# Performance work log

Measured on AMD Instinct MI355X. Metric: run time of the kernel, lower is better.

Reference implementation:

```python
import jax, jax.numpy as jnp
import numpy as np

LN_ZERO = -100000000000.0
F_, D_, C_, V_ = 250000, 4, 2, 250000
E_ = F_ * D_
CD_ = C_ ** D_


def setup_inputs() -> dict:
    key = jax.random.key(0)
    k1, k2, k3 = jax.random.split(key, 3)
    # each factor has exactly D_ incident edges, one per variable slot
    edge_f = np.repeat(np.arange(E_ // D_ * 0 + F_ * 0 + F_)[:F_], D_)  # [E]
    pos = np.tile(np.arange(D_), F_)  # variable slot of each edge within its factor
    edge_v = np.asarray(jax.random.randint(k3, (E_,), 0, V_))
    # digit of each flat factor state along each axis: digits[k, s] in [0, C)
    state = np.arange(CD_)
    digits = (state[None, :] // (C_ ** (D_ - 1 - np.arange(D_)))[:, None]) % C_  # [D, CD]
    s_p = digits[pos]  # [E, CD]: the edge's own variable state within each factor state
    # permutation indices into the broadcast-first layout [E, C, C^(D-1)]
    scatter_idx = (np.arange(E_)[:, None] * CD_ + s_p * C_ ** (D_ - 1)).reshape(-1)
    fac_states_to_var = (np.arange(E_)[:, None] * C_ + s_p).reshape(-1)
    return {
        "prv_factorToVar_messages": jax.random.normal(k1, (E_, C_), jnp.float32),
        "factor_potentials": jax.random.normal(k2, (F_,) + (C_,) * D_, jnp.float32),
        "facToVar_edge_idx": jnp.asarray(np.stack([edge_f, edge_v]), jnp.int32),
        "facStates_to_varIdx": jnp.asarray(fac_states_to_var, jnp.int32),
        "varToFactorMsg_scatter_indices": jnp.asarray(scatter_idx, jnp.int32),
        "factor_potential_masks": jnp.zeros((F_,) + (C_,) * D_, jnp.int32),
        "factorToVar_messages_masks": jnp.zeros((E_, C_), bool),
        "varToFactor_messages_masks": jnp.zeros((E_, C_), bool),
        "var_beliefs_masks": jnp.zeros((V_, C_), bool),
    }


def _mask_clamp(x, mask):
    return jnp.maximum(jnp.where(mask, LN_ZERO, x), LN_ZERO)


def reference(prv_factorToVar_messages, factor_potentials, facToVar_edge_idx,
              facStates_to_varIdx, varToFactorMsg_scatter_indices,
              factor_potential_masks, factorToVar_messages_masks,
              varToFactor_messages_masks, var_beliefs_masks):
    E, C = prv_factorToVar_messages.shape
    F = factor_potentials.shape[0]
    V = var_beliefs_masks.shape[0]
    D = factor_potentials.ndim - 1
    edge_f, edge_v = facToVar_edge_idx[0], facToVar_edge_idx[1]

    def beliefs(msgs):
        vb = _mask_clamp(jax.ops.segment_sum(msgs, edge_v, num_segments=V), var_beliefs_masks)
        v2f = _mask_clamp(vb[edge_v] - msgs, varToFactor_messages_masks)
        # expanded[e, s] = v2f[e, s_p]; source is broadcast layout [E, C, C^(D-1)]
        expanded = v2f.reshape(-1)[varToFactorMsg_scatter_indices // (C ** (D - 1))]
        expanded = expanded.reshape((E,) + (C,) * D)
        fb = jax.ops.segment_sum(expanded.reshape(E, -1), edge_f, num_segments=F)
        fb = fb.reshape(factor_potentials.shape) + factor_potentials
        fb = jnp.maximum(jnp.where(factor_potential_masks == 1, LN_ZERO, fb), LN_ZERO)
        return vb, v2f, expanded, fb

    prv_vb, prv_v2f, exp_prv_v2f, prv_fb = beliefs(prv_factorToVar_messages)

    # new factor->var messages: max-marginalize (mode='map')
    nfv = prv_fb[edge_f] - exp_prv_v2f
    nfv = nfv - jnp.max(nfv)
    flat = nfv.reshape(-1)
    seg = jnp.where(facStates_to_varIdx >= 0, facStates_to_varIdx, E * C)  # invalid -> dropped slot
    new_f2v = jax.ops.segment_max(flat, seg, num_segments=E * C + 1)[:-1].reshape(E, C)
    # normalization: logsumexp over all dims except dim 0 (here just the state axis)
    new_f2v = new_f2v - jax.nn.logsumexp(new_f2v, axis=1, keepdims=True)
    new_f2v = _mask_clamp(new_f2v, factorToVar_messages_masks)

    vb, v2f, _, fb = beliefs(new_f2v)

    damping = 0.0
    f2v = _mask_clamp(damping * prv_factorToVar_messages + (1.0 - damping) * new_f2v,
                      factorToVar_messages_masks)
    return (f2v, vb, fb)
```

## Files before the change

### kernel.cpp

```cpp
#include <hip/hip_runtime.h>
#include <hip/hip_fp16.h>
#include <math.h>
#include <string.h>

#define LN_ZERO (-100000000000.0f)

constexpr int F_ = 250000;
constexpr int V_ = 250000;
constexpr int E_ = 1000000;

constexpr int NBLK  = 256;
constexpr int PARTS = 256;
constexpr int BINS  = 977;
constexpr int CAP   = 30;
constexpr int SLICE = 3908;
constexpr int OVF_B = 1024;
constexpr int NWAVE = 16;
static_assert(PARTS * BINS >= V_, "");
static_assert((size_t)NBLK * SLICE >= E_, "");
static_assert(SLICE % 4 == 0, "");
static_assert(CAP <= 64, "segment items must fit one wave");
static_assert((size_t)NBLK * PARTS * CAP * 8 <= (size_t)F_ * 16 * 4, "buckets fit in out_fb");

static __device__ inline unsigned pack_h2(float x, float y) {
    __half2 h = __floats2half2_rn(x, y);
    unsigned u; memcpy(&u, &h, 4); return u;
}
static __device__ inline float2 unpack_h2(unsigned u) {
    __half2 h; memcpy(&h, &u, 4); return __half22float2(h);
}

__global__ __launch_bounds__(1024)
void k_ms1(const int* __restrict__ edge_v,
           const float2* __restrict__ msgs,
           const int4* __restrict__ potmask4,
           unsigned short* __restrict__ potbits,
           uint2* __restrict__ buckets,
           int* __restrict__ counts,
           uint2* __restrict__ ovf,
           int* __restrict__ ovf_counts) {
    __shared__ int cur[PARTS];
    __shared__ int ovf_cur;
    int b = blockIdx.x, tid = threadIdx.x;
    if (tid < PARTS) cur[tid] = 0;
    if (tid == 0) ovf_cur = 0;
    __syncthreads();

    int f = b * 1024 + tid;
    if (f < F_) {
        unsigned int bits = 0;
#pragma unroll
        for (int j = 0; j < 4; ++j) {
            int4 pm = potmask4[4 * f + j];
            bits |= (pm.x == 1 ? 1u : 0u) << (4 * j + 0);
            bits |= (pm.y == 1 ? 1u : 0u) << (4 * j + 1);
            bits |= (pm.z == 1 ? 1u : 0u) << (4 * j + 2);
            bits |= (pm.w == 1 ? 1u : 0u) << (4 * j + 3);
        }
        potbits[f] = (unsigned short)bits;
    }

    int ebase = b * SLICE;
    int eend = min(ebase + SLICE, E_);
    for (int e = ebase + tid; e < eend; e += 1024) {
        int v = edge_v[e];
        int p = v / BINS;
        float2 m = msgs[e];
        unsigned payload = pack_h2(m.x, m.y);
        int pos = atomicAdd(&cur[p], 1);
        if (pos < CAP) {
            buckets[((size_t)b * PARTS + p) * CAP + pos] =
                make_uint2((unsigned)(v - p * BINS), payload);
        } else {
            int op = atomicAdd(&ovf_cur, 1);
            if (op < OVF_B)
                ovf[(size_t)b * OVF_B + op] = make_uint2((unsigned)v, payload);
        }
    }
    __syncthreads();
    if (tid < PARTS) counts[tid * NBLK + b] = min(cur[tid], CAP);
    if (tid == 0) ovf_counts[b] = min(ovf_cur, OVF_B);
}

__global__ __launch_bounds__(1024)
void k_acc1(const uint2* __restrict__ buckets,
            const int* __restrict__ counts,
            const uint2* __restrict__ ovf,
            const int* __restrict__ ovf_counts,
            const unsigned short* __restrict__ vb_mask2,
            __half2* __restrict__ accP) {
    __shared__ float2 acc[BINS];
    __shared__ int ls_cnt[NBLK];
    __shared__ int ovfc[NBLK];
    int p = blockIdx.x, tid = threadIdx.x;
    int vbase = p * BINS;
    int nb = min(BINS, V_ - vbase);

    for (int j = tid; j < BINS; j += 1024) acc[j] = make_float2(0.f, 0.f);
    if (tid < NBLK) { ls_cnt[tid] = counts[p * NBLK + tid]; ovfc[tid] = ovf_counts[tid]; }
    __syncthreads();

    int wave = tid >> 6, lane = tid & 63;
    for (int b = wave; b < NBLK; b += NWAVE) {
        int n = ls_cnt[b];
        if (lane < n) {
            uint2 pr = buckets[((size_t)b * PARTS + p) * CAP + lane];
            float2 mv = unpack_h2(pr.y);
            atomicAdd(&acc[pr.x].x, mv.x);
            atomicAdd(&acc[pr.x].y, mv.y);
        }
    }
    for (int b = wave; b < NBLK; b += NWAVE) {
        int n = ovfc[b];
        for (int i = lane; i < n; i += 64) {
            uint2 pr = ovf[(size_t)b * OVF_B + i];
            int vl = (int)pr.x - vbase;
            if ((unsigned)vl < (unsigned)nb) {
                float2 mv = unpack_h2(pr.y);
                atomicAdd(&acc[vl].x, mv.x);
                atomicAdd(&acc[vl].y, mv.y);
            }
        }
    }
    __syncthreads();
    for (int j = tid; j < nb; j += 1024) {
        int v = vbase + j;
        unsigned short vbm = vb_mask2[v];
        float b0 = fmaxf((vbm & 0xff) ? LN_ZERO : acc[j].x, LN_ZERO);
        float b1 = fmaxf((vbm >> 8)   ? LN_ZERO : acc[j].y, LN_ZERO);
        accP[v] = __floats2half2_rn(b0, b1);
    }
}

__global__ __launch_bounds__(1024)
void k_fm_ms2(const float2* __restrict__ msgs,
              const int* __restrict__ edge_v,
              const __half2* __restrict__ accP,
              const float4* __restrict__ pot4,
              const unsigned short* __restrict__ potbits,
              const unsigned short* __restrict__ f2v_mask2,
              const unsigned short* __restrict__ v2f_mask2,
              float2* __restrict__ out_f2v,
              uint2* __restrict__ buckets,
              int* __restrict__ counts,
              uint2* __restrict__ ovf,
              int* __restrict__ ovf_counts) {
    __shared__ int cur[PARTS];
    __shared__ int ovf_cur;
    int b = blockIdx.x, tid = threadIdx.x;
    if (tid < PARTS) cur[tid] = 0;
    if (tid == 0) ovf_cur = 0;
    __syncthreads();

    int ebase = b * SLICE;
    int eend = min(ebase + SLICE, E_);
    for (int e = ebase + tid; e < eend; e += 1024) {
        int d = e & 3;
        int v = edge_v[e];

        float2 s = __half22float2(accP[v]);
        float2 m = msgs[e];
        unsigned short vm = v2f_mask2[e];
        float wx = fmaxf((vm & 0xff) ? LN_ZERO : (s.x - m.x), LN_ZERO);
        float wy = fmaxf((vm >> 8)   ? LN_ZERO : (s.y - m.y), LN_ZERO);

        float w0x = __shfl(wx, 0, 4), w0y = __shfl(wy, 0, 4);
        float w1x = __shfl(wx, 1, 4), w1y = __shfl(wy, 1, 4);
        float w2x = __shfl(wx, 2, 4), w2y = __shfl(wy, 2, 4);
        float w3x = __shfl(wx, 3, 4), w3y = __shfl(wy, 3, 4);

        float4 p = pot4[e];
        unsigned int pb = potbits[e >> 2] >> (4 * d);
        float A = ((d >> 1) ? w0y : w0x) + ((d & 1) ? w1y : w1x);
        float fb0 = p.x + A + w2x + w3x;
        float fb1 = p.y + A + w2x + w3y;
        float fb2 = p.z + A + w2y + w3x;
        float fb3 = p.w + A + w2y + w3y;
        fb0 = fmaxf((pb & 1u) ? LN_ZERO : fb0, LN_ZERO);
        fb1 = fmaxf((pb & 2u) ? LN_ZERO : fb1, LN_ZERO);
        fb2 = fmaxf((pb & 4u) ? LN_ZERO : fb2, LN_ZERO);
        fb3 = fmaxf((pb & 8u) ? LN_ZERO : fb3, LN_ZERO);

        float mk2_0 = fmaxf(fb0, fb1);
        float mk2_1 = fmaxf(fb2, fb3);
        float mk3_0 = fmaxf(fb0, fb2);
        float mk3_1 = fmaxf(fb1, fb3);
        float mloc  = fmaxf(mk2_0, mk2_1);

#pragma unroll
        for (int off = 1; off < 4; off <<= 1) {
            mk2_0 = fmaxf(mk2_0, __shfl_xor(mk2_0, off, 4));
            mk2_1 = fmaxf(mk2_1, __shfl_xor(mk2_1, off, 4));
            mk3_0 = fmaxf(mk3_0, __shfl_xor(mk3_0, off, 4));
            mk3_1 = fmaxf(mk3_1, __shfl_xor(mk3_1, off, 4));
        }
        float ml0 = __shfl(mloc, 0, 4);
        float ml1 = __shfl(mloc, 1, 4);
        float ml2 = __shfl(mloc, 2, 4);
        float ml3 = __shfl(mloc, 3, 4);

        float mm0, mm1;
        if (d == 0)      { mm0 = fmaxf(ml0, ml1); mm1 = fmaxf(ml2, ml3); }
        else if (d == 1) { mm0 = fmaxf(ml0, ml2); mm1 = fmaxf(ml1, ml3); }
        else if (d == 2) { mm0 = mk2_0;           mm1 = mk2_1; }
        else             { mm0 = mk3_0;           mm1 = mk3_1; }

        float raw0 = mm0 - wx;
        float raw1 = mm1 - wy;
        float mx = fmaxf(raw0, raw1);
        float lse = mx + logf(expf(raw0 - mx) + expf(raw1 - mx));
        unsigned short fm = f2v_mask2[e];
        float o0 = fmaxf((fm & 0xff) ? LN_ZERO : (raw0 - lse), LN_ZERO);
        float o1 = fmaxf((fm >> 8)   ? LN_ZERO : (raw1 - lse), LN_ZERO);
        out_f2v[e] = make_float2(o0, o1);

        int pp = v / BINS;
        unsigned payload = pack_h2(o0, o1);
        int pos = atomicAdd(&cur[pp], 1);
        if (pos < CAP) {
            buckets[((size_t)b * PARTS + pp) * CAP + pos] =
                make_uint2((unsigned)(v - pp * BINS), payload);
        } else {
            int op = atomicAdd(&ovf_cur, 1);
            if (op < OVF_B)
                ovf[(size_t)b * OVF_B + op] = make_uint2((unsigned)v, payload);
        }
    }
    __syncthreads();
    if (tid < PARTS) counts[tid * NBLK + b] = min(cur[tid], CAP);
    if (tid == 0) ovf_counts[b] = min(ovf_cur, OVF_B);
}

__global__ __launch_bounds__(1024)
void k_acc2(const uint2* __restrict__ buckets,
            const int* __restrict__ counts,
            const uint2* __restrict__ ovf,
            const int* __restrict__ ovf_counts,
            const unsigned short* __restrict__ vb_mask2,
            float2* __restrict__ out_vb,
            __half2* __restrict__ accN) {
    __shared__ float2 acc[BINS];
    __shared__ int ls_cnt[NBLK];
    __shared__ int ovfc[NBLK];
    int p = blockIdx.x, tid = threadIdx.x;
    int vbase = p * BINS;
    int nb = min(BINS, V_ - vbase);

    for (int j = tid; j < BINS; j += 1024) acc[j] = make_float2(0.f, 0.f);
    if (tid < NBLK) { ls_cnt[tid] = counts[p * NBLK + tid]; ovfc[tid] = ovf_counts[tid]; }
    __syncthreads();

    int wave = tid >> 6, lane = tid & 63;
    for (int b = wave; b < NBLK; b += NWAVE) {
        int n = ls_cnt[b];
        if (lane < n) {
            uint2 pr = buckets[((size_t)b * PARTS + p) * CAP + lane];
            float2 mv = unpack_h2(pr.y);
            atomicAdd(&acc[pr.x].x, mv.x);
            atomicAdd(&acc[pr.x].y, mv.y);
        }
    }
    for (int b = wave; b < NBLK; b += NWAVE) {
        int n = ovfc[b];
        for (int i = lane; i < n; i += 64) {
            uint2 pr = ovf[(size_t)b * OVF_B + i];
            int vl = (int)pr.x - vbase;
            if ((unsigned)vl < (unsigned)nb) {
                float2 mv = unpack_h2(pr.y);
                atomicAdd(&acc[vl].x, mv.x);
                atomicAdd(&acc[vl].y, mv.y);
            }
        }
    }
    __syncthreads();
    for (int j = tid; j < nb; j += 1024) {
        int v = vbase + j;
        unsigned short vbm = vb_mask2[v];
        float b0 = fmaxf((vbm & 0xff) ? LN_ZERO : acc[j].x, LN_ZERO);
        float b1 = fmaxf((vbm >> 8)   ? LN_ZERO : acc[j].y, LN_ZERO);
        out_vb[v] = make_float2(b0, b1);
        accN[v] = __floats2half2_rn(b0, b1);
    }
}

__global__ void k_factor_beliefs(const float2* __restrict__ new_f2v,
                                 const __half2* __restrict__ accN,
                                 const int* __restrict__ edge_v,
                                 const float4* __restrict__ pot4,
                                 const unsigned short* __restrict__ potbits,
                                 const unsigned short* __restrict__ v2f_mask2,
                                 float4* __restrict__ out_fb4) {
    int e = blockIdx.x * blockDim.x + threadIdx.x;
    if (e >= E_) return;
    int d = e & 3;

    float2 b = __half22float2(accN[edge_v[e]]);
    float2 g = new_f2v[e];
    unsigned short vm = v2f_mask2[e];
    float wx = fmaxf((vm & 0xff) ? LN_ZERO : (b.x - g.x), LN_ZERO);
    float wy = fmaxf((vm >> 8)   ? LN_ZERO : (b.y - g.y), LN_ZERO);

    float w0x = __shfl(wx, 0, 4), w0y = __shfl(wy, 0, 4);
    float w1x = __shfl(wx, 1, 4), w1y = __shfl(wy, 1, 4);
    float w2x = __shfl(wx, 2, 4), w2y = __shfl(wy, 2, 4);
    float w3x = __shfl(wx, 3, 4), w3y = __shfl(wy, 3, 4);

    float4 p = pot4[e];
    unsigned int pb = potbits[e >> 2] >> (4 * d);
    float A = ((d >> 1) ? w0y : w0x) + ((d & 1) ? w1y : w1x);
    float o0 = fmaxf((pb & 1u) ? LN_ZERO : (p.x + A + w2x + w3x), LN_ZERO);
    float o1 = fmaxf((pb & 2u) ? LN_ZERO : (p.y + A + w2x + w3y), LN_ZERO);
    float o2 = fmaxf((pb & 4u) ? LN_ZERO : (p.z + A + w2y + w3x), LN_ZERO);
    float o3 = fmaxf((pb & 8u) ? LN_ZERO : (p.w + A + w2y + w3y), LN_ZERO);
    out_fb4[e] = make_float4(o0, o1, o2, o3);
}

extern "C" void kernel_launch(void* const* d_in, const int* in_sizes, int n_in,
                              void* d_out, int out_size, void* d_ws, size_t ws_size,
                              hipStream_t stream) {
    const float* msgs     = (const float*)d_in[0];
    const float* pot      = (const float*)d_in[1];
    const int*   edge_idx = (const int*)d_in[2];
    const int*   pot_mask = (const int*)d_in[5];
    const unsigned char* f2v_mask = (const unsigned char*)d_in[6];
    const unsigned char* v2f_mask = (const unsigned char*)d_in[7];
    const unsigned char* vb_mask  = (const unsigned char*)d_in[8];

    const int* edge_v = edge_idx + E_;

    float* out      = (float*)d_out;
    float* out_f2v  = out;
    float* out_vb   = out + (size_t)E_ * 2;
    float* out_fb   = out_vb + (size_t)V_ * 2;

    uint2* buckets = (uint2*)out_fb;

    int* counts = (int*)d_ws;
    int* ovf_counts = counts + NBLK * PARTS;
    uint2* ovf = (uint2*)(ovf_counts + NBLK);
    __half2* accP = (__half2*)(ovf + (size_t)NBLK * OVF_B);
    __half2* accN = accP + V_;
    unsigned short* potbits = (unsigned short*)(accN + V_);

    const int B = 256;
    dim3 gE((E_ + B - 1) / B);

    k_ms1<<<NBLK, 1024, 0, stream>>>(edge_v, (const float2*)msgs,
                                     (const int4*)pot_mask, potbits,
                                     buckets, counts, ovf, ovf_counts);
    k_acc1<<<PARTS, 1024, 0, stream>>>(buckets, counts, ovf, ovf_counts,
                                       (const unsigned short*)vb_mask, accP);

    k_fm_ms2<<<NBLK, 1024, 0, stream>>>((const float2*)msgs, edge_v, accP,
                                        (const float4*)pot, potbits,
                                        (const unsigned short*)f2v_mask,
                                        (const unsigned short*)v2f_mask,
                                        (float2*)out_f2v,
                                        buckets, counts, ovf, ovf_counts);

    k_acc2<<<PARTS, 1024, 0, stream>>>(buckets, counts, ovf, ovf_counts,
                                       (const unsigned short*)vb_mask,
                                       (float2*)out_vb, accN);

    k_factor_beliefs<<<gE, B, 0, stream>>>((const float2*)out_f2v, accN, edge_v,
                                           (const float4*)pot, potbits,
                                           (const unsigned short*)v2f_mask,
                                           (float4*)out_fb);
}
```

Measured before the change: 75.00 us.

## Fuse five kernel launches into one cooperative kernel with grid syncs

Merges the scatter, accumulate, max-marginal, second accumulate, and factor-belief kernels into a single cooperative launch of 256 blocks of 1024 threads, with grid.sync between phases. The goal is to remove per-launch overhead and the gaps between dependent kernels. In exchange, the final factor-belief phase now runs on a fixed 256K-thread grid-stride loop instead of its own grid. Grid-wide barriers also add cost, and the launch depends on all 256 blocks being co-resident.

```diff
diff --git a/kernel.cpp b/kernel.cpp
--- a/kernel.cpp
+++ b/kernel.cpp
@@ -1,7 +1,10 @@
 #include <hip/hip_runtime.h>
+#include <hip/hip_cooperative_groups.h>
 #include <hip/hip_fp16.h>
 #include <math.h>
 #include <string.h>
+
+namespace cg = cooperative_groups;
 
 #define LN_ZERO (-100000000000.0f)
 
@@ -16,6 +19,7 @@
 constexpr int SLICE = 3908;
 constexpr int OVF_B = 1024;
 constexpr int NWAVE = 16;
+constexpr int NTHREADS = NBLK * 1024;
 static_assert(PARTS * BINS >= V_, "");
 static_assert((size_t)NBLK * SLICE >= E_, "");
 static_assert(SLICE % 4 == 0, "");
@@ -31,288 +35,260 @@
 }
 
 __global__ __launch_bounds__(1024)
-void k_ms1(const int* __restrict__ edge_v,
+void k_all(const int* __restrict__ edge_v,
            const float2* __restrict__ msgs,
            const int4* __restrict__ potmask4,
-           unsigned short* __restrict__ potbits,
-           uint2* __restrict__ buckets,
+           const float4* __restrict__ pot4,
+           const unsigned short* __restrict__ f2v_mask2,
+           const unsigned short* __restrict__ v2f_mask2,
+           const unsigned short* __restrict__ vb_mask2,
+           float2* __restrict__ out_f2v,
+           float2* __restrict__ out_vb,
+           float4* out_fb4,
+           uint2* buckets,
            int* __restrict__ counts,
            uint2* __restrict__ ovf,
-           int* __restrict__ ovf_counts) {
-    __shared__ int cur[PARTS];
-    __shared__ int ovf_cur;
-    int b = blockIdx.x, tid = threadIdx.x;
-    if (tid < PARTS) cur[tid] = 0;
-    if (tid == 0) ovf_cur = 0;
+           int* __restrict__ ovf_counts,
+           __half2* __restrict__ accP,
+           __half2* __restrict__ accN,
+           unsigned short* __restrict__ potbits) {
+    cg::grid_group grid = cg::this_grid();
+
+    __shared__ float2 s_acc[BINS];
+    __shared__ int s_ls[NBLK];
+    __shared__ int s_ovfc[NBLK];
+    __shared__ int s_cur[PARTS];
+    __shared__ int s_ovfcur;
+
+    const int b = blockIdx.x, tid = threadIdx.x;
+    const int wave = tid >> 6, lane = tid & 63;
+    const int ebase = b * SLICE;
+    const int eend = min(ebase + SLICE, E_);
+
+    if (tid < PARTS) s_cur[tid] = 0;
+    if (tid == 0) s_ovfcur = 0;
     __syncthreads();
 
-    int f = b * 1024 + tid;
-    if (f < F_) {
-        unsigned int bits = 0;
+    {
+        int f = b * 1024 + tid;
+        if (f < F_) {
+            unsigned int bits = 0;
 #pragma unroll
-        for (int j = 0; j < 4; ++j) {
-            int4 pm = potmask4[4 * f + j];
-            bits |= (pm.x == 1 ? 1u : 0u) << (4 * j + 0);
-            bits |= (pm.y == 1 ? 1u : 0u) << (4 * j + 1);
-            bits |= (pm.z == 1 ? 1u : 0u) << (4 * j + 2);
-            bits |= (pm.w == 1 ? 1u : 0u) << (4 * j + 3);
-        }
-        potbits[f] = (unsigned short)bits;
-    }
-
-    int ebase = b * SLICE;
-    int eend = min(ebase + SLICE, E_);
-    for (int e = ebase + tid; e < eend; e += 1024) {
-        int v = edge_v[e];
-        int p = v / BINS;
-        float2 m = msgs[e];
-        unsigned payload = pack_h2(m.x, m.y);
-        int pos = atomicAdd(&cur[p], 1);
-        if (pos < CAP) {
-            buckets[((size_t)b * PARTS + p) * CAP + pos] =
-                make_uint2((unsigned)(v - p * BINS), payload);
-        } else {
-            int op = atomicAdd(&ovf_cur, 1);
-            if (op < OVF_B)
-                ovf[(size_t)b * OVF_B + op] = make_uint2((unsigned)v, payload);
-        }
-    }
+            for (int j = 0; j < 4; ++j) {
+                int4 pm = potmask4[4 * f + j];
+                bits |= (pm.x == 1 ? 1u : 0u) << (4 * j + 0);
+                bits |= (pm.y == 1 ? 1u : 0u) << (4 * j + 1);
+                bits |= (pm.z == 1 ? 1u : 0u) << (4 * j + 2);
+                bits |= (pm.w == 1 ? 1u : 0u) << (4 * j + 3);
+            }
+            potbits[f] = (unsigned short)bits;
+        }
+        for (int e = ebase + tid; e < eend; e += 1024) {
+            int v = edge_v[e];
+            int p = v / BINS;
+            float2 m = msgs[e];
+            unsigned payload = pack_h2(m.x, m.y);
+            int pos = atomicAdd(&s_cur[p], 1);
+            if (pos < CAP) {
+                buckets[((size_t)b * PARTS + p) * CAP + pos] =
+                    make_uint2((unsigned)(v - p * BINS), payload);
+            } else {
+                int op = atomicAdd(&s_ovfcur, 1);
+                if (op < OVF_B)
+                    ovf[(size_t)b * OVF_B + op] = make_uint2((unsigned)v, payload);
+            }
+        }
+        __syncthreads();
+        if (tid < PARTS) counts[tid * NBLK + b] = min(s_cur[tid], CAP);
+        if (tid == 0) ovf_counts[b] = min(s_ovfcur, OVF_B);
+    }
+    grid.sync();
+
+    {
+        const int p = b;
+        int vbase = p * BINS;
+        int nb = min(BINS, V_ - vbase);
+        for (int j = tid; j < BINS; j += 1024) s_acc[j] = make_float2(0.f, 0.f);
+        if (tid < NBLK) { s_ls[tid] = counts[p * NBLK + tid]; s_ovfc[tid] = ovf_counts[tid]; }
+        __syncthreads();
+        for (int s = wave; s < NBLK; s += NWAVE) {
+            int n = s_ls[s];
+            if (lane < n) {
+                uint2 pr = buckets[((size_t)s * PARTS + p) * CAP + lane];
+                float2 mv = unpack_h2(pr.y);
+                atomicAdd(&s_acc[pr.x].x, mv.x);
+                atomicAdd(&s_acc[pr.x].y, mv.y);
+            }
+        }
+        for (int s = wave; s < NBLK; s += NWAVE) {
+            int n = s_ovfc[s];
+            for (int i = lane; i < n; i += 64) {
+                uint2 pr = ovf[(size_t)s * OVF_B + i];
+                int vl = (int)pr.x - vbase;
+                if ((unsigned)vl < (unsigned)nb) {
+                    float2 mv = unpack_h2(pr.y);
+                    atomicAdd(&s_acc[vl].x, mv.x);
+                    atomicAdd(&s_acc[vl].y, mv.y);
+                }
+            }
+        }
+        __syncthreads();
+        for (int j = tid; j < nb; j += 1024) {
+            int v = vbase + j;
+            unsigned short vbm = vb_mask2[v];
+            float b0 = fmaxf((vbm & 0xff) ? LN_ZERO : s_acc[j].x, LN_ZERO);
+            float b1 = fmaxf((vbm >> 8)   ? LN_ZERO : s_acc[j].y, LN_ZERO);
+            accP[v] = __floats2half2_rn(b0, b1);
+        }
+    }
+    grid.sync();
+
+    if (tid < PARTS) s_cur[tid] = 0;
+    if (tid == 0) s_ovfcur = 0;
     __syncthreads();
-    if (tid < PARTS) counts[tid * NBLK + b] = min(cur[tid], CAP);
-    if (tid == 0) ovf_counts[b] = min(ovf_cur, OVF_B);
-}
-
-__global__ __launch_bounds__(1024)
-void k_acc1(const uint2* __restrict__ buckets,
-            const int* __restrict__ counts,
-            const uint2* __restrict__ ovf,
-            const int* __restrict__ ovf_counts,
-            const unsigned short* __restrict__ vb_mask2,
-            __half2* __restrict__ accP) {
-    __shared__ float2 acc[BINS];
-    __shared__ int ls_cnt[NBLK];
-    __shared__ int ovfc[NBLK];
-    int p = blockIdx.x, tid = threadIdx.x;
-    int vbase = p * BINS;
-    int nb = min(BINS, V_ - vbase);
-
-    for (int j = tid; j < BINS; j += 1024) acc[j] = make_float2(0.f, 0.f);
-    if (tid < NBLK) { ls_cnt[tid] = counts[p * NBLK + tid]; ovfc[tid] = ovf_counts[tid]; }
-    __syncthreads();
-
-    int wave = tid >> 6, lane = tid & 63;
-    for (int b = wave; b < NBLK; b += NWAVE) {
-        int n = ls_cnt[b];
-        if (lane < n) {
-            uint2 pr = buckets[((size_t)b * PARTS + p) * CAP + lane];
-            float2 mv = unpack_h2(pr.y);
-            atomicAdd(&acc[pr.x].x, mv.x);
-            atomicAdd(&acc[pr.x].y, mv.y);
-        }
-    }
-    for (int b = wave; b < NBLK; b += NWAVE) {
-        int n = ovfc[b];
-        for (int i = lane; i < n; i += 64) {
-            uint2 pr = ovf[(size_t)b * OVF_B + i];
-            int vl = (int)pr.x - vbase;
-            if ((unsigned)vl < (unsigned)nb) {
+    {
+        for (int e = ebase + tid; e < eend; e += 1024) {
+            int d = e & 3;
+            int v = edge_v[e];
+
+            float2 s = __half22float2(accP[v]);
+            float2 m = msgs[e];
+            unsigned short vm = v2f_mask2[e];
+            float wx = fmaxf((vm & 0xff) ? LN_ZERO : (s.x - m.x), LN_ZERO);
+            float wy = fmaxf((vm >> 8)   ? LN_ZERO : (s.y - m.y), LN_ZERO);
+
+            float w0x = __shfl(wx, 0, 4), w0y = __shfl(wy, 0, 4);
+            float w1x = __shfl(wx, 1, 4), w1y = __shfl(wy, 1, 4);
+            float w2x = __shfl(wx, 2, 4), w2y = __shfl(wy, 2, 4);
+            float w3x = __shfl(wx, 3, 4), w3y = __shfl(wy, 3, 4);
+
+            float4 p = pot4[e];
+            unsigned int pb = potbits[e >> 2] >> (4 * d);
+            float A = ((d >> 1) ? w0y : w0x) + ((d & 1) ? w1y : w1x);
+            float fb0 = p.x + A + w2x + w3x;
+            float fb1 = p.y + A + w2x + w3y;
+            float fb2 = p.z + A + w2y + w3x;
+            float fb3 = p.w + A + w2y + w3y;
+            fb0 = fmaxf((pb & 1u) ? LN_ZERO : fb0, LN_ZERO);
+            fb1 = fmaxf((pb & 2u) ? LN_ZERO : fb1, LN_ZERO);
+            fb2 = fmaxf((pb & 4u) ? LN_ZERO : fb2, LN_ZERO);
+            fb3 = fmaxf((pb & 8u) ? LN_ZERO : fb3, LN_ZERO);
+
+            float mk2_0 = fmaxf(fb0, fb1);
+            float mk2_1 = fmaxf(fb2, fb3);
+            float mk3_0 = fmaxf(fb0, fb2);
+            float mk3_1 = fmaxf(fb1, fb3);
+            float mloc  = fmaxf(mk2_0, mk2_1);
+
+#pragma unroll
+            for (int off = 1; off < 4; off <<= 1) {
+                mk2_0 = fmaxf(mk2_0, __shfl_xor(mk2_0, off, 4));
+                mk2_1 = fmaxf(mk2_1, __shfl_xor(mk2_1, off, 4));
+                mk3_0 = fmaxf(mk3_0, __shfl_xor(mk3_0, off, 4));
+                mk3_1 = fmaxf(mk3_1, __shfl_xor(mk3_1, off, 4));
+            }
+            float ml0 = __shfl(mloc, 0, 4);
+            float ml1 = __shfl(mloc, 1, 4);
+            float ml2 = __shfl(mloc, 2, 4);
+            float ml3 = __shfl(mloc, 3, 4);
+
+            float mm0, mm1;
+            if (d == 0)      { mm0 = fmaxf(ml0, ml1); mm1 = fmaxf(ml2, ml3); }
+            else if (d == 1) { mm0 = fmaxf(ml0, ml2); mm1 = fmaxf(ml1, ml3); }
+            else if (d == 2) { mm0 = mk2_0;           mm1 = mk2_1; }
+            else             { mm0 = mk3_0;           mm1 = mk3_1; }
+
+            float raw0 = mm0 - wx;
+            float raw1 = mm1 - wy;
+            float mx = fmaxf(raw0, raw1);
+            float lse = mx + logf(expf(raw0 - mx) + expf(raw1 - mx));
+            unsigned short fm = f2v_mask2[e];
+            float o0 = fmaxf((fm & 0xff) ? LN_ZERO : (raw0 - lse), LN_ZERO);
+            float o1 = fmaxf((fm >> 8)   ? LN_ZERO : (raw1 - lse), LN_ZERO);
+            out_f2v[e] = make_float2(o0, o1);
+
+            int pp = v / BINS;
+            unsigned payload = pack_h2(o0, o1);
+            int pos = atomicAdd(&s_cur[pp], 1);
+            if (pos < CAP) {
+                buckets[((size_t)b * PARTS + pp) * CAP + pos] =
+                    make_uint2((unsigned)(v - pp * BINS), payload);
+            } else {
+                int op = atomicAdd(&s_ovfcur, 1);
+                if (op < OVF_B)
+                    ovf[(size_t)b * OVF_B + op] = make_uint2((unsigned)v, payload);
+            }
+        }
+        __syncthreads();
+        if (tid < PARTS) counts[tid * NBLK + b] = min(s_cur[tid], CAP);
+        if (tid == 0) ovf_counts[b] = min(s_ovfcur, OVF_B);
+    }
+    grid.sync();
+
+    {
+        const int p = b;
+        int vbase = p * BINS;
+        int nb = min(BINS, V_ - vbase);
+        for (int j = tid; j < BINS; j += 1024) s_acc[j] = make_float2(0.f, 0.f);
+        if (tid < NBLK) { s_ls[tid] = counts[p * NBLK + tid]; s_ovfc[tid] = ovf_counts[tid]; }
+        __syncthreads();
+        for (int s = wave; s < NBLK; s += NWAVE) {
+            int n = s_ls[s];
+            if (lane < n) {
+                uint2 pr = buckets[((size_t)s * PARTS + p) * CAP + lane];
                 float2 mv = unpack_h2(pr.y);
-                atomicAdd(&acc[vl].x, mv.x);
-                atomicAdd(&acc[vl].y, mv.y);
-            }
-        }
-    }
-    __syncthreads();
-    for (int j = tid; j < nb; j += 1024) {
-        int v = vbase + j;
-        unsigned short vbm = vb_mask2[v];
-        float b0 = fmaxf((vbm & 0xff) ? LN_ZERO : acc[j].x, LN_ZERO);
-        float b1 = fmaxf((vbm >> 8)   ? LN_ZERO : acc[j].y, LN_ZERO);
-        accP[v] = __floats2half2_rn(b0, b1);
-    }
-}
-
-__global__ __launch_bounds__(1024)
-void k_fm_ms2(const float2* __restrict__ msgs,
-              const int* __restrict__ edge_v,
-              const __half2* __restrict__ accP,
-              const float4* __restrict__ pot4,
-              const unsigned short* __restrict__ potbits,
-              const unsigned short* __restrict__ f2v_mask2,
-              const unsigned short* __restrict__ v2f_mask2,
-              float2* __restrict__ out_f2v,
-              uint2* __restrict__ buckets,
-              int* __restrict__ counts,
-              uint2* __restrict__ ovf,
-              int* __restrict__ ovf_counts) {
-    __shared__ int cur[PARTS];
-    __shared__ int ovf_cur;
-    int b = blockIdx.x, tid = threadIdx.x;
-    if (tid < PARTS) cur[tid] = 0;
-    if (tid == 0) ovf_cur = 0;
-    __syncthreads();
-
-    int ebase = b * SLICE;
-    int eend = min(ebase + SLICE, E_);
-    for (int e = ebase + tid; e < eend; e += 1024) {
-        int d = e & 3;
-        int v = edge_v[e];
-
-        float2 s = __half22float2(accP[v]);
-        float2 m = msgs[e];
-        unsigned short vm = v2f_mask2[e];
-        float wx = fmaxf((vm & 0xff) ? LN_ZERO : (s.x - m.x), LN_ZERO);
-        float wy = fmaxf((vm >> 8)   ? LN_ZERO : (s.y - m.y), LN_ZERO);
-
-        float w0x = __shfl(wx, 0, 4), w0y = __shfl(wy, 0, 4);
-        float w1x = __shfl(wx, 1, 4), w1y = __shfl(wy, 1, 4);
-        float w2x = __shfl(wx, 2, 4), w2y = __shfl(wy, 2, 4);
-        float w3x = __shfl(wx, 3, 4), w3y = __shfl(wy, 3, 4);
-
-        float4 p = pot4[e];
-        unsigned int pb = potbits[e >> 2] >> (4 * d);
-        float A = ((d >> 1) ? w0y : w0x) + ((d & 1) ? w1y : w1x);
-        float fb0 = p.x + A + w2x + w3x;
-        float fb1 = p.y + A + w2x + w3y;
-        float fb2 = p.z + A + w2y + w3x;
-        float fb3 = p.w + A + w2y + w3y;
-        fb0 = fmaxf((pb & 1u) ? LN_ZERO : fb0, LN_ZERO);
-        fb1 = fmaxf((pb & 2u) ? LN_ZERO : fb1, LN_ZERO);
-        fb2 = fmaxf((pb & 4u) ? LN_ZERO : fb2, LN_ZERO);
-        fb3 = fmaxf((pb & 8u) ? LN_ZERO : fb3, LN_ZERO);
-
-        float mk2_0 = fmaxf(fb0, fb1);
-        float mk2_1 = fmaxf(fb2, fb3);
-        float mk3_0 = fmaxf(fb0, fb2);
-        float mk3_1 = fmaxf(fb1, fb3);
-        float mloc  = fmaxf(mk2_0, mk2_1);
-
-#pragma unroll
-        for (int off = 1; off < 4; off <<= 1) {
-            mk2_0 = fmaxf(mk2_0, __shfl_xor(mk2_0, off, 4));
-            mk2_1 = fmaxf(mk2_1, __shfl_xor(mk2_1, off, 4));
-            mk3_0 = fmaxf(mk3_0, __shfl_xor(mk3_0, off, 4));
-            mk3_1 = fmaxf(mk3_1, __shfl_xor(mk3_1, off, 4));
-        }
-        float ml0 = __shfl(mloc, 0, 4);
-        float ml1 = __shfl(mloc, 1, 4);
-        float ml2 = __shfl(mloc, 2, 4);
-        float ml3 = __shfl(mloc, 3, 4);
-
-        float mm0, mm1;
-        if (d == 0)      { mm0 = fmaxf(ml0, ml1); mm1 = fmaxf(ml2, ml3); }
-        else if (d == 1) { mm0 = fmaxf(ml0, ml2); mm1 = fmaxf(ml1, ml3); }
-        else if (d == 2) { mm0 = mk2_0;           mm1 = mk2_1; }
-        else             { mm0 = mk3_0;           mm1 = mk3_1; }
-
-        float raw0 = mm0 - wx;
-        float raw1 = mm1 - wy;
-        float mx = fmaxf(raw0, raw1);
-        float lse = mx + logf(expf(raw0 - mx) + expf(raw1 - mx));
-        unsigned short fm = f2v_mask2[e];
-        float o0 = fmaxf((fm & 0xff) ? LN_ZERO : (raw0 - lse), LN_ZERO);
-        float o1 = fmaxf((fm >> 8)   ? LN_ZERO : (raw1 - lse), LN_ZERO);
-        out_f2v[e] = make_float2(o0, o1);
-
-        int pp = v / BINS;
-        unsigned payload = pack_h2(o0, o1);
-        int pos = atomicAdd(&cur[pp], 1);
-        if (pos < CAP) {
-            buckets[((size_t)b * PARTS + pp) * CAP + pos] =
-                make_uint2((unsigned)(v - pp * BINS), payload);
-        } else {
-            int op = atomicAdd(&ovf_cur, 1);
-            if (op < OVF_B)
-                ovf[(size_t)b * OVF_B + op] = make_uint2((unsigned)v, payload);
-        }
-    }
-    __syncthreads();
-    if (tid < PARTS) counts[tid * NBLK + b] = min(cur[tid], CAP);
-    if (tid == 0) ovf_counts[b] = min(ovf_cur, OVF_B);
-}
-
-__global__ __launch_bounds__(1024)
-void k_acc2(const uint2* __restrict__ buckets,
-            const int* __restrict__ counts,
-            const uint2* __restrict__ ovf,
-            const int* __restrict__ ovf_counts,
-            const unsigned short* __restrict__ vb_mask2,
-            float2* __restrict__ out_vb,
-            __half2* __restrict__ accN) {
-    __shared__ float2 acc[BINS];
-    __shared__ int ls_cnt[NBLK];
-    __shared__ int ovfc[NBLK];
-    int p = blockIdx.x, tid = threadIdx.x;
-    int vbase = p * BINS;
-    int nb = min(BINS, V_ - vbase);
-
-    for (int j = tid; j < BINS; j += 1024) acc[j] = make_float2(0.f, 0.f);
-    if (tid < NBLK) { ls_cnt[tid] = counts[p * NBLK + tid]; ovfc[tid] = ovf_counts[tid]; }
-    __syncthreads();
-
-    int wave = tid >> 6, lane = tid & 63;
-    for (int b = wave; b < NBLK; b += NWAVE) {
-        int n = ls_cnt[b];
-        if (lane < n) {
-            uint2 pr = buckets[((size_t)b * PARTS + p) * CAP + lane];
-            float2 mv = unpack_h2(pr.y);
-            atomicAdd(&acc[pr.x].x, mv.x);
-            atomicAdd(&acc[pr.x].y, mv.y);
-        }
-    }
-    for (int b = wave; b < NBLK; b += NWAVE) {
-        int n = ovfc[b];
-        for (int i = lane; i < n; i += 64) {
-            uint2 pr = ovf[(size_t)b * OVF_B + i];
-            int vl = (int)pr.x - vbase;
-            if ((unsigned)vl < (unsigned)nb) {
-                float2 mv = unpack_h2(pr.y);
-                atomicAdd(&acc[vl].x, mv.x);
-                atomicAdd(&acc[vl].y, mv.y);
-            }
-        }
-    }
-    __syncthreads();
-    for (int j = tid; j < nb; j += 1024) {
-        int v = vbase + j;
-        unsigned short vbm = vb_mask2[v];
-        float b0 = fmaxf((vbm & 0xff) ? LN_ZERO : acc[j].x, LN_ZERO);
-        float b1 = fmaxf((vbm >> 8)   ? LN_ZERO : acc[j].y, LN_ZERO);
-        out_vb[v] = make_float2(b0, b1);
-        accN[v] = __floats2half2_rn(b0, b1);
-    }
-}
-
-__global__ void k_factor_beliefs(const float2* __restrict__ new_f2v,
-                                 const __half2* __restrict__ accN,
-                                 const int* __restrict__ edge_v,
-                                 const float4* __restrict__ pot4,
-                                 const unsigned short* __restrict__ potbits,
-                                 const unsigned short* __restrict__ v2f_mask2,
-                                 float4* __restrict__ out_fb4) {
-    int e = blockIdx.x * blockDim.x + threadIdx.x;
-    if (e >= E_) return;
-    int d = e & 3;
-
-    float2 b = __half22float2(accN[edge_v[e]]);
-    float2 g = new_f2v[e];
-    unsigned short vm = v2f_mask2[e];
-    float wx = fmaxf((vm & 0xff) ? LN_ZERO : (b.x - g.x), LN_ZERO);
-    float wy = fmaxf((vm >> 8)   ? LN_ZERO : (b.y - g.y), LN_ZERO);
-
-    float w0x = __shfl(wx, 0, 4), w0y = __shfl(wy, 0, 4);
-    float w1x = __shfl(wx, 1, 4), w1y = __shfl(wy, 1, 4);
-    float w2x = __shfl(wx, 2, 4), w2y = __shfl(wy, 2, 4);
-    float w3x = __shfl(wx, 3, 4), w3y = __shfl(wy, 3, 4);
-
-    float4 p = pot4[e];
-    unsigned int pb = potbits[e >> 2] >> (4 * d);
-    float A = ((d >> 1) ? w0y : w0x) + ((d & 1) ? w1y : w1x);
-    float o0 = fmaxf((pb & 1u) ? LN_ZERO : (p.x + A + w2x + w3x), LN_ZERO);
-    float o1 = fmaxf((pb & 2u) ? LN_ZERO : (p.y + A + w2x + w3y), LN_ZERO);
-    float o2 = fmaxf((pb & 4u) ? LN_ZERO : (p.z + A + w2y + w3x), LN_ZERO);
-    float o3 = fmaxf((pb & 8u) ? LN_ZERO : (p.w + A + w2y + w3y), LN_ZERO);
-    out_fb4[e] = make_float4(o0, o1, o2, o3);
+                atomicAdd(&s_acc[pr.x].x, mv.x);
+                atomicAdd(&s_acc[pr.x].y, mv.y);
+            }
+        }
+        for (int s = wave; s < NBLK; s += NWAVE) {
+            int n = s_ovfc[s];
+            for (int i = lane; i < n; i += 64) {
+                uint2 pr = ovf[(size_t)s * OVF_B + i];
+                int vl = (int)pr.x - vbase;
+                if ((unsigned)vl < (unsigned)nb) {
+                    float2 mv = unpack_h2(pr.y);
+                    atomicAdd(&s_acc[vl].x, mv.x);
+                    atomicAdd(&s_acc[vl].y, mv.y);
+                }
+            }
+        }
+        __syncthreads();
+        for (int j = tid; j < nb; j += 1024) {
+            int v = vbase + j;
+            unsigned short vbm = vb_mask2[v];
+            float b0 = fmaxf((vbm & 0xff) ? LN_ZERO : s_acc[j].x, LN_ZERO);
+            float b1 = fmaxf((vbm >> 8)   ? LN_ZERO : s_acc[j].y, LN_ZERO);
+            out_vb[v] = make_float2(b0, b1);
+            accN[v] = __floats2half2_rn(b0, b1);
+        }
+    }
+    grid.sync();
+
+    {
+        for (int e = b * 1024 + tid; e < E_; e += NTHREADS) {
+            int d = e & 3;
+            float2 bb = __half22float2(accN[edge_v[e]]);
+            float2 g = out_f2v[e];
+            unsigned short vm = v2f_mask2[e];
+            float wx = fmaxf((vm & 0xff) ? LN_ZERO : (bb.x - g.x), LN_ZERO);
+            float wy = fmaxf((vm >> 8)   ? LN_ZERO : (bb.y - g.y), LN_ZERO);
+
+            float w0x = __shfl(wx, 0, 4), w0y = __shfl(wy, 0, 4);
+            float w1x = __shfl(wx, 1, 4), w1y = __shfl(wy, 1, 4);
+            float w2x = __shfl(wx, 2, 4), w2y = __shfl(wy, 2, 4);
+            float w3x = __shfl(wx, 3, 4), w3y = __shfl(wy, 3, 4);
+
+            float4 p = pot4[e];
+            unsigned int pb = potbits[e >> 2] >> (4 * d);
+            float A = ((d >> 1) ? w0y : w0x) + ((d & 1) ? w1y : w1x);
+            float o0 = fmaxf((pb & 1u) ? LN_ZERO : (p.x + A + w2x + w3x), LN_ZERO);
+            float o1 = fmaxf((pb & 2u) ? LN_ZERO : (p.y + A + w2x + w3y), LN_ZERO);
+            float o2 = fmaxf((pb & 4u) ? LN_ZERO : (p.z + A + w2y + w3x), LN_ZERO);
+            float o3 = fmaxf((pb & 8u) ? LN_ZERO : (p.w + A + w2y + w3y), LN_ZERO);
+            out_fb4[e] = make_float4(o0, o1, o2, o3);
+        }
+    }
 }
 
 extern "C" void kernel_launch(void* const* d_in, const int* in_sizes, int n_in,
@@ -342,28 +318,23 @@
     __half2* accN = accP + V_;
     unsigned short* potbits = (unsigned short*)(accN + V_);
 
-    const int B = 256;
-    dim3 gE((E_ + B - 1) / B);
-
-    k_ms1<<<NBLK, 1024, 0, stream>>>(edge_v, (const float2*)msgs,
-                                     (const int4*)pot_mask, potbits,
-                                     buckets, counts, ovf, ovf_counts);
-    k_acc1<<<PARTS, 1024, 0, stream>>>(buckets, counts, ovf, ovf_counts,
-                                       (const unsigned short*)vb_mask, accP);
-
-    k_fm_ms2<<<NBLK, 1024, 0, stream>>>((const float2*)msgs, edge_v, accP,
-                                        (const float4*)pot, potbits,
-                                        (const unsigned short*)f2v_mask,
-                                        (const unsigned short*)v2f_mask,
-                                        (float2*)out_f2v,
-                                        buckets, counts, ovf, ovf_counts);
-
-    k_acc2<<<PARTS, 1024, 0, stream>>>(buckets, counts, ovf, ovf_counts,
-                                       (const unsigned short*)vb_mask,
-                                       (float2*)out_vb, accN);
-
-    k_factor_beliefs<<<gE, B, 0, stream>>>((const float2*)out_f2v, accN, edge_v,
-                                           (const float4*)pot, potbits,
-                                           (const unsigned short*)v2f_mask,
-                                           (float4*)out_fb);
+    const float2* msgs2 = (const float2*)msgs;
+    const int4* potmask4 = (const int4*)pot_mask;
+    const float4* pot4 = (const float4*)pot;
+    const unsigned short* f2v_mask2 = (const unsigned short*)f2v_mask;
+    const unsigned short* v2f_mask2 = (const unsigned short*)v2f_mask;
+    const unsigned short* vb_mask2 = (const unsigned short*)vb_mask;
+    float2* out_f2v2 = (float2*)out_f2v;
+    float2* out_vb2 = (float2*)out_vb;
+    float4* out_fb4 = (float4*)out_fb;
+
+    void* args[] = {
+        (void*)&edge_v, (void*)&msgs2, (void*)&potmask4, (void*)&pot4,
+        (void*)&f2v_mask2, (void*)&v2f_mask2, (void*)&vb_mask2,
+        (void*)&out_f2v2, (void*)&out_vb2, (void*)&out_fb4,
+        (void*)&buckets, (void*)&counts, (void*)&ovf, (void*)&ovf_counts,
+        (void*)&accP, (void*)&accN, (void*)&potbits,
+    };
+    hipLaunchCooperativeKernel((const void*)k_all, dim3(NBLK), dim3(1024),
+                               args, 0, stream);
 }
```

After: 215.3 us. 187% more time.

## Reuse first-pass bucket slots so second scatter skips atomic binning

Applied to the files above, without the earlier changes.

The first binning kernel now records, for each edge, the bucket or overflow slot it was assigned. The factor-max kernel reuses that rank instead of rebinning with shared-memory atomics. This lets it run as a flat grid of 256-thread blocks rather than 256 persistent 1024-thread blocks, removing the atomics and the block-wide syncs. The cost is writing and reading a 4-byte-per-edge rank array, and it relies on both passes using the same edge-to-variable mapping so the counts from the first pass stay valid.

```diff
diff --git a/kernel.cpp b/kernel.cpp
--- a/kernel.cpp
+++ b/kernel.cpp
@@ -38,7 +38,8 @@
            uint2* __restrict__ buckets,
            int* __restrict__ counts,
            uint2* __restrict__ ovf,
-           int* __restrict__ ovf_counts) {
+           int* __restrict__ ovf_counts,
+           unsigned* __restrict__ rank) {
     __shared__ int cur[PARTS];
     __shared__ int ovf_cur;
     int b = blockIdx.x, tid = threadIdx.x;
@@ -69,12 +70,18 @@
         unsigned payload = pack_h2(m.x, m.y);
         int pos = atomicAdd(&cur[p], 1);
         if (pos < CAP) {
-            buckets[((size_t)b * PARTS + p) * CAP + pos] =
-                make_uint2((unsigned)(v - p * BINS), payload);
+            unsigned gi = (unsigned)(((size_t)b * PARTS + p) * CAP + pos);
+            buckets[gi] = make_uint2((unsigned)(v - p * BINS), payload);
+            rank[e] = gi;
         } else {
             int op = atomicAdd(&ovf_cur, 1);
-            if (op < OVF_B)
-                ovf[(size_t)b * OVF_B + op] = make_uint2((unsigned)v, payload);
+            if (op < OVF_B) {
+                unsigned oi = (unsigned)(b * OVF_B + op);
+                ovf[oi] = make_uint2((unsigned)v, payload);
+                rank[e] = 0x80000000u | oi;
+            } else {
+                rank[e] = 0xFFFFFFFFu;
+            }
         }
     }
     __syncthreads();
@@ -132,103 +139,87 @@
     }
 }
 
-__global__ __launch_bounds__(1024)
-void k_fm_ms2(const float2* __restrict__ msgs,
-              const int* __restrict__ edge_v,
-              const __half2* __restrict__ accP,
-              const float4* __restrict__ pot4,
-              const unsigned short* __restrict__ potbits,
-              const unsigned short* __restrict__ f2v_mask2,
-              const unsigned short* __restrict__ v2f_mask2,
-              float2* __restrict__ out_f2v,
-              uint2* __restrict__ buckets,
-              int* __restrict__ counts,
-              uint2* __restrict__ ovf,
-              int* __restrict__ ovf_counts) {
-    __shared__ int cur[PARTS];
-    __shared__ int ovf_cur;
-    int b = blockIdx.x, tid = threadIdx.x;
-    if (tid < PARTS) cur[tid] = 0;
-    if (tid == 0) ovf_cur = 0;
-    __syncthreads();
-
-    int ebase = b * SLICE;
-    int eend = min(ebase + SLICE, E_);
-    for (int e = ebase + tid; e < eend; e += 1024) {
-        int d = e & 3;
-        int v = edge_v[e];
-
-        float2 s = __half22float2(accP[v]);
-        float2 m = msgs[e];
-        unsigned short vm = v2f_mask2[e];
-        float wx = fmaxf((vm & 0xff) ? LN_ZERO : (s.x - m.x), LN_ZERO);
-        float wy = fmaxf((vm >> 8)   ? LN_ZERO : (s.y - m.y), LN_ZERO);
-
-        float w0x = __shfl(wx, 0, 4), w0y = __shfl(wy, 0, 4);
-        float w1x = __shfl(wx, 1, 4), w1y = __shfl(wy, 1, 4);
-        float w2x = __shfl(wx, 2, 4), w2y = __shfl(wy, 2, 4);
-        float w3x = __shfl(wx, 3, 4), w3y = __shfl(wy, 3, 4);
-
-        float4 p = pot4[e];
-        unsigned int pb = potbits[e >> 2] >> (4 * d);
-        float A = ((d >> 1) ? w0y : w0x) + ((d & 1) ? w1y : w1x);
-        float fb0 = p.x + A + w2x + w3x;
-        float fb1 = p.y + A + w2x + w3y;
-        float fb2 = p.z + A + w2y + w3x;
-        float fb3 = p.w + A + w2y + w3y;
-        fb0 = fmaxf((pb & 1u) ? LN_ZERO : fb0, LN_ZERO);
-        fb1 = fmaxf((pb & 2u) ? LN_ZERO : fb1, LN_ZERO);
-        fb2 = fmaxf((pb & 4u) ? LN_ZERO : fb2, LN_ZERO);
-        fb3 = fmaxf((pb & 8u) ? LN_ZERO : fb3, LN_ZERO);
-
-        float mk2_0 = fmaxf(fb0, fb1);
-        float mk2_1 = fmaxf(fb2, fb3);
-        float mk3_0 = fmaxf(fb0, fb2);
-        float mk3_1 = fmaxf(fb1, fb3);
-        float mloc  = fmaxf(mk2_0, mk2_1);
+__global__ void k_fm(const float2* __restrict__ msgs,
+                     const int* __restrict__ edge_v,
+                     const unsigned* __restrict__ rank,
+                     const __half2* __restrict__ accP,
+                     const float4* __restrict__ pot4,
+                     const unsigned short* __restrict__ potbits,
+                     const unsigned short* __restrict__ f2v_mask2,
+                     const unsigned short* __restrict__ v2f_mask2,
+                     float2* __restrict__ out_f2v,
+                     uint2* __restrict__ buckets,
+                     uint2* __restrict__ ovf) {
+    int e = blockIdx.x * blockDim.x + threadIdx.x;
+    if (e >= E_) return;
+    int d = e & 3;
+    int v = edge_v[e];
+
+    float2 s = __half22float2(accP[v]);
+    float2 m = msgs[e];
+    unsigned short vm = v2f_mask2[e];
+    float wx = fmaxf((vm & 0xff) ? LN_ZERO : (s.x - m.x), LN_ZERO);
+    float wy = fmaxf((vm >> 8)   ? LN_ZERO : (s.y - m.y), LN_ZERO);
+
+    float w0x = __shfl(wx, 0, 4), w0y = __shfl(wy, 0, 4);
+    float w1x = __shfl(wx, 1, 4), w1y = __shfl(wy, 1, 4);
+    float w2x = __shfl(wx, 2, 4), w2y = __shfl(wy, 2, 4);
+    float w3x = __shfl(wx, 3, 4), w3y = __shfl(wy, 3, 4);
+
+    float4 p = pot4[e];
+    unsigned int pb = potbits[e >> 2] >> (4 * d);
+    float A = ((d >> 1) ? w0y : w0x) + ((d & 1) ? w1y : w1x);
+    float fb0 = p.x + A + w2x + w3x;
+    float fb1 = p.y + A + w2x + w3y;
+    float fb2 = p.z + A + w2y + w3x;
+    float fb3 = p.w + A + w2y + w3y;
+    fb0 = fmaxf((pb & 1u) ? LN_ZERO : fb0, LN_ZERO);
+    fb1 = fmaxf((pb & 2u) ? LN_ZERO : fb1, LN_ZERO);
+    fb2 = fmaxf((pb & 4u) ? LN_ZERO : fb2, LN_ZERO);
+    fb3 = fmaxf((pb & 8u) ? LN_ZERO : fb3, LN_ZERO);
+
+    float mk2_0 = fmaxf(fb0, fb1);
+    float mk2_1 = fmaxf(fb2, fb3);
+    float mk3_0 = fmaxf(fb0, fb2);
+    float mk3_1 = fmaxf(fb1, fb3);
+    float mloc  = fmaxf(mk2_0, mk2_1);
 
 #pragma unroll
-        for (int off = 1; off < 4; off <<= 1) {
-            mk2_0 = fmaxf(mk2_0, __shfl_xor(mk2_0, off, 4));
-            mk2_1 = fmaxf(mk2_1, __shfl_xor(mk2_1, off, 4));
-            mk3_0 = fmaxf(mk3_0, __shfl_xor(mk3_0, off, 4));
-            mk3_1 = fmaxf(mk3_1, __shfl_xor(mk3_1, off, 4));
-        }
-        float ml0 = __shfl(mloc, 0, 4);
-        float ml1 = __shfl(mloc, 1, 4);
-        float ml2 = __shfl(mloc, 2, 4);
-        float ml3 = __shfl(mloc, 3, 4);
-
-        float mm0, mm1;
-        if (d == 0)      { mm0 = fmaxf(ml0, ml1); mm1 = fmaxf(ml2, ml3); }
-        else if (d == 1) { mm0 = fmaxf(ml0, ml2); mm1 = fmaxf(ml1, ml3); }
-        else if (d == 2) { mm0 = mk2_0;           mm1 = mk2_1; }
-        else             { mm0 = mk3_0;           mm1 = mk3_1; }
-
-        float raw0 = mm0 - wx;
-        float raw1 = mm1 - wy;
-        float mx = fmaxf(raw0, raw1);
-        float lse = mx + logf(expf(raw0 - mx) + expf(raw1 - mx));
-        unsigned short fm = f2v_mask2[e];
-        float o0 = fmaxf((fm & 0xff) ? LN_ZERO : (raw0 - lse), LN_ZERO);
-        float o1 = fmaxf((fm >> 8)   ? LN_ZERO : (raw1 - lse), LN_ZERO);
-        out_f2v[e] = make_float2(o0, o1);
-
+    for (int off = 1; off < 4; off <<= 1) {
+        mk2_0 = fmaxf(mk2_0, __shfl_xor(mk2_0, off, 4));
+        mk2_1 = fmaxf(mk2_1, __shfl_xor(mk2_1, off, 4));
+        mk3_0 = fmaxf(mk3_0, __shfl_xor(mk3_0, off, 4));
+        mk3_1 = fmaxf(mk3_1, __shfl_xor(mk3_1, off, 4));
+    }
+    float ml0 = __shfl(mloc, 0, 4);
+    float ml1 = __shfl(mloc, 1, 4);
+    float ml2 = __shfl(mloc, 2, 4);
+    float ml3 = __shfl(mloc, 3, 4);
+
+    float mm0, mm1;
+    if (d == 0)      { mm0 = fmaxf(ml0, ml1); mm1 = fmaxf(ml2, ml3); }
+    else if (d == 1) { mm0 = fmaxf(ml0, ml2); mm1 = fmaxf(ml1, ml3); }
+    else if (d == 2) { mm0 = mk2_0;           mm1 = mk2_1; }
+    else             { mm0 = mk3_0;           mm1 = mk3_1; }
+
+    float raw0 = mm0 - wx;
+    float raw1 = mm1 - wy;
+    float mx = fmaxf(raw0, raw1);
+    float lse = mx + logf(expf(raw0 - mx) + expf(raw1 - mx));
+    unsigned short fm = f2v_mask2[e];
+    float o0 = fmaxf((fm & 0xff) ? LN_ZERO : (raw0 - lse), LN_ZERO);
+    float o1 = fmaxf((fm >> 8)   ? LN_ZERO : (raw1 - lse), LN_ZERO);
+    out_f2v[e] = make_float2(o0, o1);
+
+    unsigned r = rank[e];
+    unsigned payload = pack_h2(o0, o1);
+    if (r == 0xFFFFFFFFu) {
+    } else if (r & 0x80000000u) {
+        ovf[r & 0x7FFFFFFFu] = make_uint2((unsigned)v, payload);
+    } else {
         int pp = v / BINS;
-        unsigned payload = pack_h2(o0, o1);
-        int pos = atomicAdd(&cur[pp], 1);
-        if (pos < CAP) {
-            buckets[((size_t)b * PARTS + pp) * CAP + pos] =
-                make_uint2((unsigned)(v - pp * BINS), payload);
-        } else {
-            int op = atomicAdd(&ovf_cur, 1);
-            if (op < OVF_B)
-                ovf[(size_t)b * OVF_B + op] = make_uint2((unsigned)v, payload);
-        }
-    }
-    __syncthreads();
-    if (tid < PARTS) counts[tid * NBLK + b] = min(cur[tid], CAP);
-    if (tid == 0) ovf_counts[b] = min(ovf_cur, OVF_B);
+        buckets[r] = make_uint2((unsigned)(v - pp * BINS), payload);
+    }
 }
 
 __global__ __launch_bounds__(1024)
@@ -341,22 +332,22 @@
     __half2* accP = (__half2*)(ovf + (size_t)NBLK * OVF_B);
     __half2* accN = accP + V_;
     unsigned short* potbits = (unsigned short*)(accN + V_);
+    unsigned* rank = (unsigned*)(potbits + F_);
 
     const int B = 256;
     dim3 gE((E_ + B - 1) / B);
 
     k_ms1<<<NBLK, 1024, 0, stream>>>(edge_v, (const float2*)msgs,
                                      (const int4*)pot_mask, potbits,
-                                     buckets, counts, ovf, ovf_counts);
+                                     buckets, counts, ovf, ovf_counts, rank);
     k_acc1<<<PARTS, 1024, 0, stream>>>(buckets, counts, ovf, ovf_counts,
                                        (const unsigned short*)vb_mask, accP);
 
-    k_fm_ms2<<<NBLK, 1024, 0, stream>>>((const float2*)msgs, edge_v, accP,
-                                        (const float4*)pot, potbits,
-                                        (const unsigned short*)f2v_mask,
-                                        (const unsigned short*)v2f_mask,
-                                        (float2*)out_f2v,
-                                        buckets, counts, ovf, ovf_counts);
+    k_fm<<<gE, B, 0, stream>>>((const float2*)msgs, edge_v, rank, accP,
+                               (const float4*)pot, potbits,
+                               (const unsigned short*)f2v_mask,
+                               (const unsigned short*)v2f_mask,
+                               (float2*)out_f2v, buckets, ovf);
 
     k_acc2<<<PARTS, 1024, 0, stream>>>(buckets, counts, ovf, ovf_counts,
                                        (const unsigned short*)vb_mask,
```

After: 77.34 us. 3.1% more time.
